# Performance work log

Measured on AMD Instinct MI355X. Metric: run time of the kernel, lower is better.

Reference implementation:

```python
import jax, jax.numpy as jnp
import numpy as np

K0, KMIN, KMAX = 4, 3, 6
SIZE = 7
SR = 2  # fixed sampling ratio (torchvision default is adaptive; fixed 2 is the standard jit-friendly reference)
LEVELS = (3, 4, 5, 6)


def yxhw_to_tlbr(b):
    y, x, h, w = b[:, 0], b[:, 1], b[:, 2], b[:, 3]
    return jnp.stack([y - h / 2, x - w / 2, y + h / 2, x + w / 2], axis=1)


def compute_level_ids(boxes):
    areas = boxes[:, 2] * boxes[:, 3]
    k = jnp.floor(K0 + jnp.log2(jnp.sqrt(areas) / 224.0))
    return jnp.clip(k, KMIN, KMAX).astype(jnp.int32)


def roi_align(feat, rois, img_ids, out_size, sr):
    # feat: [B,C,H,W]; rois: [N,4] as (x1,y1,x2,y2) in feature coords (aligned=False semantics)
    B, C, H, W = feat.shape
    x1, y1, x2, y2 = rois[:, 0], rois[:, 1], rois[:, 2], rois[:, 3]
    roi_w = jnp.maximum(x2 - x1, 1.0)
    roi_h = jnp.maximum(y2 - y1, 1.0)
    bin_w = roi_w / out_size
    bin_h = roi_h / out_size
    # per-bin sample offsets: [out, sr]
    off = jnp.arange(out_size, dtype=feat.dtype)[:, None] + (jnp.arange(sr, dtype=feat.dtype) + 0.5) / sr
    ys = y1[:, None, None] + off[None] * bin_h[:, None, None]  # [N,Oy,Sy]
    xs = x1[:, None, None] + off[None] * bin_w[:, None, None]  # [N,Ox,Sx]
    y = ys[:, :, :, None, None]  # [N,Oy,Sy,1,1]
    x = xs[:, None, None, :, :]  # [N,1,1,Ox,Sx]
    valid = (y >= -1.0) & (y <= H) & (x >= -1.0) & (x <= W)  # [N,Oy,Sy,Ox,Sx]
    yc = jnp.clip(y, 0.0, H - 1.0)
    xc = jnp.clip(x, 0.0, W - 1.0)
    yl = jnp.floor(yc).astype(jnp.int32)
    xl = jnp.floor(xc).astype(jnp.int32)
    yh = jnp.minimum(yl + 1, H - 1)
    xh = jnp.minimum(xl + 1, W - 1)
    ly = yc - yl
    lx = xc - xl
    hy = 1.0 - ly
    hx = 1.0 - lx
    img = img_ids[:, None, None, None, None]

    def g(yy, xx):
        # advanced indexing: -> [N,Oy,Sy,Ox,Sx,C]
        return feat[img, :, yy, xx]

    val = ((hy * hx)[..., None] * g(yl, xl)
           + (hy * lx)[..., None] * g(yl, xh)
           + (ly * hx)[..., None] * g(yh, xl)
           + (ly * lx)[..., None] * g(yh, xh))
    val = jnp.where(valid[..., None], val, 0.0)
    pooled = val.mean(axis=(2, 4))  # average over (Sy,Sx) -> [N,Oy,Ox,C]
    return pooled.transpose(0, 3, 1, 2)  # [N,C,Oy,Ox]


def setup_inputs() -> dict:
    key = jax.random.key(0)
    ks = jax.random.split(key, 7)
    B, C, N = 4, 256, 1024
    yx = jax.random.uniform(ks[0], (N, 2), dtype=jnp.float32) * 1024.0
    hw = jax.random.uniform(ks[1], (N, 2), dtype=jnp.float32) * 480.0 + 32.0
    boxes = jnp.concatenate([yx, hw], axis=1)  # (yc, xc, h, w)
    image_ids = jax.random.randint(ks[2], (N,), 0, B, dtype=jnp.int32)
    fmap3 = jax.random.normal(ks[3], (B, C, 128, 128), dtype=jnp.float32)
    fmap4 = jax.random.normal(ks[4], (B, C, 64, 64), dtype=jnp.float32)
    fmap5 = jax.random.normal(ks[5], (B, C, 32, 32), dtype=jnp.float32)
    fmap6 = jax.random.normal(ks[6], (B, C, 16, 16), dtype=jnp.float32)
    return {"fmap3": fmap3, "fmap4": fmap4, "fmap5": fmap5, "fmap6": fmap6,
            "boxes": boxes, "image_ids": image_ids}


def reference(fmap3, fmap4, fmap5, fmap6, boxes, image_ids):
    level_ids = compute_level_ids(boxes)
    tlbr = yxhw_to_tlbr(boxes)  # passed to roi_align as-is, matching the torch code
    out = None
    for lvl, fmap in zip(LEVELS, (fmap3, fmap4, fmap5, fmap6)):
        stride = float(2 ** lvl)
        out_l = roi_align(fmap, tlbr / stride, image_ids, SIZE, SR)
        mask = (level_ids == lvl)[:, None, None, None]
        sel = jnp.where(mask, out_l, 0.0)
        out = sel if out is None else out + sel
    return out  # [N, C, SIZE, SIZE] in original box order
```

## Files before the change

kernel.cpp:

```cpp
#include <hip/hip_runtime.h>
#include <hip/hip_bf16.h>

static constexpr size_t B3 = 0;
static constexpr size_t B4 = (size_t)4 * 256 * 16384;
static constexpr size_t B5 = B4 + (size_t)4 * 256 * 4096;
static constexpr size_t B6 = B5 + (size_t)4 * 256 * 1024;
static constexpr size_t WS_ELEMS = B6 + (size_t)4 * 256 * 256;

__global__ __launch_bounds__(256) void transpose_nchw_nhwc_bf16(
    const float* __restrict__ f3, const float* __restrict__ f4,
    const float* __restrict__ f5, const float* __restrict__ f6,
    __hip_bfloat16* __restrict__ ws)
{
    __shared__ float tile[64][65];
    const int z   = blockIdx.z;
    const int lvl = z >> 2;
    const int b   = z & 3;
    const float* in; int H; size_t base;
    if      (lvl == 0) { in = f3; H = 128; base = B3; }
    else if (lvl == 1) { in = f4; H = 64;  base = B4; }
    else if (lvl == 2) { in = f5; H = 32;  base = B5; }
    else               { in = f6; H = 16;  base = B6; }
    const int HW  = H * H;
    const int hw0 = blockIdx.x * 64;
    if (hw0 >= HW) return;
    const int c0  = blockIdx.y * 64;
    const int tx  = threadIdx.x & 63;
    const int ty  = threadIdx.x >> 6;

    const float* inp = in + ((size_t)b * 256 + c0) * (size_t)HW + hw0;
    #pragma unroll
    for (int i = 0; i < 16; ++i) {
        const int cl = ty + 4 * i;
        tile[cl][tx] = inp[(size_t)cl * HW + tx];
    }
    __syncthreads();
    __hip_bfloat16* outp = ws + base + ((size_t)b * HW + hw0) * 256 + c0;
    #pragma unroll
    for (int i = 0; i < 16; ++i) {
        const int hl = ty + 4 * i;
        outp[(size_t)hl * 256 + tx] = __float2bfloat16(tile[tx][hl]);
    }
}

__device__ __forceinline__ float bf_lo(unsigned u) { return __uint_as_float(u << 16); }
__device__ __forceinline__ float bf_hi(unsigned u) { return __uint_as_float(u & 0xffff0000u); }

__global__ __launch_bounds__(256) void roi_gather_nhwc_bf16(
    const unsigned* __restrict__ ws, const float* __restrict__ boxes,
    const int* __restrict__ img_ids, float* __restrict__ out)
{
    __shared__ float lds[49][129];
    __shared__ float rW[14][2];
    __shared__ int   rO[14][2];
    __shared__ float cW[14][2];
    __shared__ int   cO[14][2];

    const int n    = blockIdx.x;
    const int c0   = blockIdx.y * 128;
    const int t    = threadIdx.x;
    const int lane = t & 63;
    const int wv   = t >> 6;

    const float by = boxes[n * 4 + 0];
    const float bx = boxes[n * 4 + 1];
    const float bh = boxes[n * 4 + 2];
    const float bw = boxes[n * 4 + 3];

    float kf = floorf(4.0f + log2f(sqrtf(bh * bw) / 224.0f));
    kf = fminf(fmaxf(kf, 3.0f), 6.0f);
    const int lvl = (int)kf;

    int H; size_t base;
    if      (lvl == 3) { H = 128; base = B3; }
    else if (lvl == 4) { H = 64;  base = B4; }
    else if (lvl == 5) { H = 32;  base = B5; }
    else               { H = 16;  base = B6; }
    const float inv_stride = 1.0f / (float)(1 << lvl);
    const float Hf = (float)H;

    const float tY = (by - bh * 0.5f) * inv_stride;
    const float lX = (bx - bw * 0.5f) * inv_stride;
    const float bY = (by + bh * 0.5f) * inv_stride;
    const float rX = (bx + bw * 0.5f) * inv_stride;
    const float binA = fmaxf(bY - tY, 1.0f) * (1.0f / 7.0f);
    const float binB = fmaxf(rX - lX, 1.0f) * (1.0f / 7.0f);

    if (lane < 14 && wv < 2) {
        const int a = lane;
        const float off = (float)(a >> 1) + 0.25f + 0.5f * (float)(a & 1);
        if (wv == 0) {
            const float rc = lX + off * binB;
            const bool v = (rc >= -1.0f) && (rc <= Hf);
            const float yc = fminf(fmaxf(rc, 0.0f), Hf - 1.0f);
            const int yl = (int)yc;
            const int yh = min(yl + 1, H - 1);
            const float ly = yc - (float)yl;
            rW[a][0] = v ? 1.0f - ly : 0.0f;
            rW[a][1] = v ? ly : 0.0f;
            rO[a][0] = yl * H * 128;
            rO[a][1] = yh * H * 128;
        } else {
            const float cc = tY + off * binA;
            const bool v = (cc >= -1.0f) && (cc <= Hf);
            const float xc = fminf(fmaxf(cc, 0.0f), Hf - 1.0f);
            const int xl = (int)xc;
            const int xh = min(xl + 1, H - 1);
            const float lx = xc - (float)xl;
            cW[a][0] = v ? 1.0f - lx : 0.0f;
            cW[a][1] = v ? lx : 0.0f;
            cO[a][0] = xl * 128;
            cO[a][1] = xh * 128;
        }
    }
    __syncthreads();

    const int img = img_ids[n];
    const unsigned* fb = ws + (base >> 1) + (size_t)img * (size_t)(H * H) * 128
                       + (size_t)(c0 >> 1) + lane;

    for (int p = wv; p < 49; p += 4) {
        const int a0 = (p / 7) * 2;
        const int b0 = (p % 7) * 2;
        float accx = 0.0f, accy = 0.0f;
        #pragma unroll
        for (int s1 = 0; s1 < 2; ++s1) {
            const float hy = rW[a0 + s1][0], lyw = rW[a0 + s1][1];
            const int oy0 = rO[a0 + s1][0], oy1 = rO[a0 + s1][1];
            #pragma unroll
            for (int s2 = 0; s2 < 2; ++s2) {
                const float hx = cW[b0 + s2][0], lxw = cW[b0 + s2][1];
                const int ox0 = cO[b0 + s2][0], ox1 = cO[b0 + s2][1];
                const unsigned u00 = fb[oy0 + ox0];
                const unsigned u01 = fb[oy0 + ox1];
                const unsigned u10 = fb[oy1 + ox0];
                const unsigned u11 = fb[oy1 + ox1];
                const float w00 = hy * hx, w01 = hy * lxw;
                const float w10 = lyw * hx, w11 = lyw * lxw;
                accx += w00 * bf_lo(u00) + w01 * bf_lo(u01)
                      + w10 * bf_lo(u10) + w11 * bf_lo(u11);
                accy += w00 * bf_hi(u00) + w01 * bf_hi(u01)
                      + w10 * bf_hi(u10) + w11 * bf_hi(u11);
            }
        }
        lds[p][2 * lane]     = accx * 0.25f;
        lds[p][2 * lane + 1] = accy * 0.25f;
    }
    __syncthreads();

    float* op = out + ((size_t)n * 256 + c0 + wv * 32) * 49;
    if (lane < 49) {
        for (int k = 0; k < 32; ++k) {
            op[(size_t)k * 49 + lane] = lds[lane][wv * 32 + k];
        }
    }
}

__global__ __launch_bounds__(256) void roi_align_fallback(
    const float* __restrict__ f3, const float* __restrict__ f4,
    const float* __restrict__ f5, const float* __restrict__ f6,
    const float* __restrict__ boxes, const int* __restrict__ img_ids,
    float* __restrict__ out)
{
    const int n  = blockIdx.x;
    const int cg = blockIdx.y;
    const int t  = threadIdx.x;

    const float by = boxes[n * 4 + 0];
    const float bx = boxes[n * 4 + 1];
    const float bh = boxes[n * 4 + 2];
    const float bw = boxes[n * 4 + 3];

    float kf = floorf(4.0f + log2f(sqrtf(bh * bw) / 224.0f));
    kf = fminf(fmaxf(kf, 3.0f), 6.0f);
    const int lvl = (int)kf;

    const float* feat;
    int H;
    if      (lvl == 3) { feat = f3; H = 128; }
    else if (lvl == 4) { feat = f4; H = 64;  }
    else if (lvl == 5) { feat = f5; H = 32;  }
    else               { feat = f6; H = 16;  }

    const float inv_stride = 1.0f / (float)(1 << lvl);
    const float tY = (by - bh * 0.5f) * inv_stride;
    const float lX = (bx - bw * 0.5f) * inv_stride;
    const float bY = (by + bh * 0.5f) * inv_stride;
    const float rX = (bx + bw * 0.5f) * inv_stride;
    const float binA = fmaxf(bY - tY, 1.0f) / 7.0f;
    const float binB = fmaxf(rX - lX, 1.0f) / 7.0f;

    const int p   = t >> 2;
    const int s1  = (t >> 1) & 1;
    const int s2  = t & 1;
    const int ii  = p / 7;
    const int jj  = p % 7;
    const bool active = (t < 196);

    const float rc = lX + ((float)ii + ((float)s1 + 0.5f) * 0.5f) * binB;
    const float cc = tY + ((float)jj + ((float)s2 + 0.5f) * 0.5f) * binA;
    const float Hf = (float)H;
    const bool valid = active && (rc >= -1.0f) && (rc <= Hf) &&
                       (cc >= -1.0f) && (cc <= Hf);

    const float yc = fminf(fmaxf(rc, 0.0f), Hf - 1.0f);
    const float xc = fminf(fmaxf(cc, 0.0f), Hf - 1.0f);
    int yl = (int)floorf(yc);
    int xl = (int)floorf(xc);
    int yh = min(yl + 1, H - 1);
    int xh = min(xl + 1, H - 1);
    const float ly = yc - (float)yl;
    const float lx = xc - (float)xl;
    const float hy = 1.0f - ly;
    const float hx = 1.0f - lx;
    float w00 = hy * hx, w01 = hy * lx, w10 = ly * hx, w11 = ly * lx;
    if (!valid) { w00 = w01 = w10 = w11 = 0.0f; yl = xl = yh = xh = 0; }

    const int img = img_ids[n];
    const int HH  = H * H;
    const int c0  = cg * 64;
    const float* basep = feat + (size_t)(img * 256 + c0) * (size_t)HH;
    const int o00 = yl * H + xl, o01 = yl * H + xh;
    const int o10 = yh * H + xl, o11 = yh * H + xh;

    float* outp = out + ((size_t)n * 256 + c0) * 49 + p;
    #pragma unroll 4
    for (int c = 0; c < 64; ++c) {
        float v = w00 * basep[o00] + w01 * basep[o01]
                + w10 * basep[o10] + w11 * basep[o11];
        v += __shfl_xor(v, 1);
        v += __shfl_xor(v, 2);
        if (active && (t & 3) == 0) outp[(size_t)c * 49] = v * 0.25f;
        basep += HH;
    }
}

extern "C" void kernel_launch(void* const* d_in, const int* in_sizes, int n_in,
                              void* d_out, int out_size, void* d_ws, size_t ws_size,
                              hipStream_t stream)
{
    const float* f3      = (const float*)d_in[0];
    const float* f4      = (const float*)d_in[1];
    const float* f5      = (const float*)d_in[2];
    const float* f6      = (const float*)d_in[3];
    const float* boxes   = (const float*)d_in[4];
    const int*   img_ids = (const int*)d_in[5];
    float* outp          = (float*)d_out;
    const int N = in_sizes[5];

    if (ws_size >= WS_ELEMS * sizeof(__hip_bfloat16)) {
        __hip_bfloat16* ws = (__hip_bfloat16*)d_ws;
        dim3 tgrid(256, 4, 16);
        transpose_nchw_nhwc_bf16<<<tgrid, 256, 0, stream>>>(f3, f4, f5, f6, ws);
        dim3 ggrid(N, 2);
        roi_gather_nhwc_bf16<<<ggrid, 256, 0, stream>>>((const unsigned*)d_ws, boxes, img_ids, outp);
    } else {
        dim3 grid(N, 4);
        roi_align_fallback<<<grid, 256, 0, stream>>>(f3, f4, f5, f6, boxes, img_ids, outp);
    }
}
```

Baseline: 57.78 us.

## Gather all 256 channels per block with 8-byte bf16 loads

Each ROI is now handled by one 512-thread block that covers all 256 channels, where before two blocks each covered 128. Every lane loads a uint2, which is four bf16 channels, instead of a 32-bit pair. This halves the number of load instructions and removes the duplicate per-ROI setup that the two channel-half blocks both did. In exchange, the LDS footprint grows to about 51KB and the grid holds half as many blocks, which may reduce occupancy. The final transpose also needs a permuted channel index because of the strided channel layout in LDS.

```diff
diff --git a/kernel.cpp b/kernel.cpp
--- a/kernel.cpp
+++ b/kernel.cpp
@@ -46,18 +46,17 @@
 __device__ __forceinline__ float bf_lo(unsigned u) { return __uint_as_float(u << 16); }
 __device__ __forceinline__ float bf_hi(unsigned u) { return __uint_as_float(u & 0xffff0000u); }
 
-__global__ __launch_bounds__(256) void roi_gather_nhwc_bf16(
-    const unsigned* __restrict__ ws, const float* __restrict__ boxes,
+__global__ __launch_bounds__(512) void roi_gather_nhwc_bf16(
+    const uint2* __restrict__ ws, const float* __restrict__ boxes,
     const int* __restrict__ img_ids, float* __restrict__ out)
 {
-    __shared__ float lds[49][129];
+    __shared__ float lds[49][261];
     __shared__ float rW[14][2];
     __shared__ int   rO[14][2];
     __shared__ float cW[14][2];
     __shared__ int   cO[14][2];
 
     const int n    = blockIdx.x;
-    const int c0   = blockIdx.y * 128;
     const int t    = threadIdx.x;
     const int lane = t & 63;
     const int wv   = t >> 6;
@@ -98,8 +97,8 @@
             const float ly = yc - (float)yl;
             rW[a][0] = v ? 1.0f - ly : 0.0f;
             rW[a][1] = v ? ly : 0.0f;
-            rO[a][0] = yl * H * 128;
-            rO[a][1] = yh * H * 128;
+            rO[a][0] = yl * H * 64;
+            rO[a][1] = yh * H * 64;
         } else {
             const float cc = tY + off * binA;
             const bool v = (cc >= -1.0f) && (cc <= Hf);
@@ -109,20 +108,19 @@
             const float lx = xc - (float)xl;
             cW[a][0] = v ? 1.0f - lx : 0.0f;
             cW[a][1] = v ? lx : 0.0f;
-            cO[a][0] = xl * 128;
-            cO[a][1] = xh * 128;
+            cO[a][0] = xl * 64;
+            cO[a][1] = xh * 64;
         }
     }
     __syncthreads();
 
     const int img = img_ids[n];
-    const unsigned* fb = ws + (base >> 1) + (size_t)img * (size_t)(H * H) * 128
-                       + (size_t)(c0 >> 1) + lane;
-
-    for (int p = wv; p < 49; p += 4) {
+    const uint2* fb = ws + (base >> 2) + (size_t)img * (size_t)(H * H) * 64 + lane;
+
+    for (int p = wv; p < 49; p += 8) {
         const int a0 = (p / 7) * 2;
         const int b0 = (p % 7) * 2;
-        float accx = 0.0f, accy = 0.0f;
+        float a0c = 0.0f, a1c = 0.0f, a2c = 0.0f, a3c = 0.0f;
         #pragma unroll
         for (int s1 = 0; s1 < 2; ++s1) {
             const float hy = rW[a0 + s1][0], lyw = rW[a0 + s1][1];
@@ -131,27 +129,36 @@
             for (int s2 = 0; s2 < 2; ++s2) {
                 const float hx = cW[b0 + s2][0], lxw = cW[b0 + s2][1];
                 const int ox0 = cO[b0 + s2][0], ox1 = cO[b0 + s2][1];
-                const unsigned u00 = fb[oy0 + ox0];
-                const unsigned u01 = fb[oy0 + ox1];
-                const unsigned u10 = fb[oy1 + ox0];
-                const unsigned u11 = fb[oy1 + ox1];
+                const uint2 u00 = fb[oy0 + ox0];
+                const uint2 u01 = fb[oy0 + ox1];
+                const uint2 u10 = fb[oy1 + ox0];
+                const uint2 u11 = fb[oy1 + ox1];
                 const float w00 = hy * hx, w01 = hy * lxw;
                 const float w10 = lyw * hx, w11 = lyw * lxw;
-                accx += w00 * bf_lo(u00) + w01 * bf_lo(u01)
-                      + w10 * bf_lo(u10) + w11 * bf_lo(u11);
-                accy += w00 * bf_hi(u00) + w01 * bf_hi(u01)
-                      + w10 * bf_hi(u10) + w11 * bf_hi(u11);
+                a0c += w00 * bf_lo(u00.x) + w01 * bf_lo(u01.x)
+                     + w10 * bf_lo(u10.x) + w11 * bf_lo(u11.x);
+                a1c += w00 * bf_hi(u00.x) + w01 * bf_hi(u01.x)
+                     + w10 * bf_hi(u10.x) + w11 * bf_hi(u11.x);
+                a2c += w00 * bf_lo(u00.y) + w01 * bf_lo(u01.y)
+                     + w10 * bf_lo(u10.y) + w11 * bf_lo(u11.y);
+                a3c += w00 * bf_hi(u00.y) + w01 * bf_hi(u01.y)
+                     + w10 * bf_hi(u10.y) + w11 * bf_hi(u11.y);
             }
         }
-        lds[p][2 * lane]     = accx * 0.25f;
-        lds[p][2 * lane + 1] = accy * 0.25f;
+        lds[p][lane]       = a0c * 0.25f;
+        lds[p][lane + 64]  = a1c * 0.25f;
+        lds[p][lane + 128] = a2c * 0.25f;
+        lds[p][lane + 192] = a3c * 0.25f;
     }
     __syncthreads();
 
-    float* op = out + ((size_t)n * 256 + c0 + wv * 32) * 49;
+    float* op = out + (size_t)n * 256 * 49;
     if (lane < 49) {
+        #pragma unroll 4
         for (int k = 0; k < 32; ++k) {
-            op[(size_t)k * 49 + lane] = lds[lane][wv * 32 + k];
+            const int c = wv * 32 + k;
+            const int pc = (c >> 2) + 64 * (c & 3);
+            op[(size_t)c * 49 + lane] = lds[lane][pc];
         }
     }
 }
@@ -249,11 +256,11 @@
     const int N = in_sizes[5];
 
     if (ws_size >= WS_ELEMS * sizeof(__hip_bfloat16)) {
-        __hip_bfloat16* ws = (__hip_bfloat16*)d_ws;
         dim3 tgrid(256, 4, 16);
-        transpose_nchw_nhwc_bf16<<<tgrid, 256, 0, stream>>>(f3, f4, f5, f6, ws);
-        dim3 ggrid(N, 2);
-        roi_gather_nhwc_bf16<<<ggrid, 256, 0, stream>>>((const unsigned*)d_ws, boxes, img_ids, outp);
+        transpose_nchw_nhwc_bf16<<<tgrid, 256, 0, stream>>>(
+            f3, f4, f5, f6, (__hip_bfloat16*)d_ws);
+        roi_gather_nhwc_bf16<<<N, 512, 0, stream>>>(
+            (const uint2*)d_ws, boxes, img_ids, outp);
     } else {
         dim3 grid(N, 4);
         roi_align_fallback<<<grid, 256, 0, stream>>>(f3, f4, f5, f6, boxes, img_ids, outp);
```

Result: slower. 60.63 us (+4.9%).
